# Optimization experiments

Hardware: AMD Instinct MI355X
Metric: run time of the kernel (lower is better)

Reference implementation:

```python
import jax, jax.numpy as jnp
import numpy as np

N_HEADS = 4
EMBED = 128
KDIM = EMBED // N_HEADS  # 32
FFH = 512
EPS = 1e-5


def _layer_norm_global(x):
    # PDP-N2S 'layer' norm: normalize over ALL of (nodes, features) per sample,
    # torch .var() is unbiased (ddof=1)
    mean = jnp.mean(x, axis=(1, 2), keepdims=True)
    var = jnp.var(x, axis=(1, 2), keepdims=True, ddof=1)
    return (x - mean) / jnp.sqrt(var + EPS)


def setup_inputs() -> dict:
    key = jax.random.key(0)
    ks = jax.random.split(key, 12)
    B, N = 8, 1024
    u = lambda k, shape, fan: jax.random.uniform(k, shape, jnp.float32, -1.0 / np.sqrt(fan), 1.0 / np.sqrt(fan))
    return {
        "input1": jax.random.normal(ks[0], (B, N, EMBED), jnp.float32),
        "input2": jax.random.normal(ks[1], (N_HEADS, B, N, N), jnp.float32),
        "W_query": u(ks[2], (N_HEADS, EMBED, KDIM), KDIM),
        "W_key": u(ks[3], (N_HEADS, EMBED, KDIM), KDIM),
        "W_val": u(ks[4], (N_HEADS, EMBED, KDIM), KDIM),
        "W_out": u(ks[5], (N_HEADS, KDIM, EMBED), EMBED),
        "Ws1": u(ks[6], (8, 8), 8),   # score_aggr layer 1, stored (in,out)
        "bs1": u(ks[7], (8,), 8),
        "Ws2": u(ks[8], (8, 4), 4),
        "bs2": u(ks[9], (4,), 4),
        "W_ff1": u(ks[10], (EMBED, FFH), FFH),  # stored (in,out), no bias
        "W_ff2": u(ks[11], (FFH, EMBED), EMBED),
    }


def reference(input1, input2, W_query, W_key, W_val, W_out, Ws1, bs1, Ws2, bs2, W_ff1, W_ff2):
    h = input1  # [B,N,E]
    # per-head projections: [H,B,N,K]
    Q = jnp.einsum('bne,hek->hbnk', h, W_query)
    K = jnp.einsum('bne,hek->hbnk', h, W_key)
    V = jnp.einsum('bne,hek->hbnk', h, W_val)
    # compatibility: 4 QK^T heads concatenated with 4 auxiliary score heads -> [8,B,N,N]
    compat = jnp.concatenate([jnp.einsum('hbnk,hbmk->hbnm', Q, K), input2], axis=0)
    # tiny per-element MLP across the 8-channel head axis -> 4 heads
    x = jnp.moveaxis(compat, 0, -1)                     # [B,N,N,8]
    x = jax.nn.relu(x @ Ws1 + bs1) @ Ws2 + bs2          # [B,N,N,4]
    attn = jax.nn.softmax(jnp.moveaxis(x, -1, 0), axis=-1)  # [4,B,N,N]
    heads = jnp.einsum('hbnm,hbmk->hbnk', attn, V)      # [H,B,N,K]
    out = jnp.einsum('hbnk,hke->bne', heads, W_out)     # [B,N,E]
    out1 = _layer_norm_global(out + h)
    # FF sublayer + norm
    ff = jax.nn.relu(out1 @ W_ff1) @ W_ff2
    out1 = _layer_norm_global(ff + out1)
    return (out1, input2)
```

## Files before the change

kernel.cpp:

```cpp
#include <hip/hip_runtime.h>
#include <hip/hip_bf16.h>

typedef __hip_bfloat16 bf16;

static constexpr int HN  = 4;
static constexpr int NB  = 8;
static constexpr int SEQ = 1024;
static constexpr int EMB = 128;
static constexpr int KD  = 32;
static constexpr int FFH = 512;
static constexpr int ROWS = NB * SEQ;
static constexpr float EPS = 1e-5f;

__device__ __forceinline__ float b2f(bf16 x){ return __bfloat162float(x); }

__device__ __forceinline__ float ldx(const void* p, size_t i, int f32){
    return f32 ? ((const float*)p)[i] : b2f(((const bf16*)p)[i]);
}

__device__ __forceinline__ float probe_max(const unsigned int* w, int nwords, int t){
    float mx = 0.f;
    for (int i = t; i < nwords; i += 256) {
        float v = fabsf(__uint_as_float(w[i] << 16));
        if (!(v <= 1e4f)) v = 1e30f;
        mx = fmaxf(mx, v);
    }
    return mx;
}

__global__ __launch_bounds__(256) void detect_kernel(
    const unsigned int* in1, const unsigned int* in2,
    const unsigned int* wq,  const unsigned int* wk, const unsigned int* wv,
    const unsigned int* wo,  const unsigned int* ws1, const unsigned int* bs1,
    const unsigned int* ws2, const unsigned int* bs2,
    const unsigned int* wf1, const unsigned int* wf2, int* __restrict__ flags)
{
    __shared__ float red[4];
    const int b = blockIdx.x, t = threadIdx.x;
    float mx = 0.f;
    if      (b == 0) mx = probe_max(in1, 4096, t);
    else if (b == 1) mx = probe_max(in2, 4096, t);
    else if (b == 2) mx = probe_max(wq, 4096, t);
    else if (b == 3) mx = probe_max(wk, 4096, t);
    else if (b == 4) mx = probe_max(wv, 4096, t);
    else if (b == 5) mx = probe_max(wo, 4096, t);
    else if (b == 6) {
        mx = fmaxf(probe_max(ws1, 32, t), probe_max(bs1, 4, t));
        mx = fmaxf(mx, fmaxf(probe_max(ws2, 16, t), probe_max(bs2, 2, t)));
    }
    else if (b == 7) mx = probe_max(wf1, 4096, t);
    else             mx = probe_max(wf2, 4096, t);

    #pragma unroll
    for (int off = 32; off >= 1; off >>= 1) mx = fmaxf(mx, __shfl_xor(mx, off));
    if ((t & 63) == 0) red[t >> 6] = mx;
    __syncthreads();
    if (t == 0) {
        mx = fmaxf(fmaxf(red[0], red[1]), fmaxf(red[2], red[3]));
        flags[b] = (mx > 1e4f) ? 1 : 0;
    }
}

__global__ __launch_bounds__(256) void convert_kernel(
    const void* in1, const void* Wq, const void* Wk, const void* Wv, const void* Wo,
    const void* Ws1, const void* bs1, const void* Ws2, const void* bs2,
    const void* Wf1, const void* Wf2,
    float* __restrict__ h32, float* __restrict__ Wt, float* __restrict__ Wot,
    float* __restrict__ W1t, float* __restrict__ W2t, float* __restrict__ mlp32,
    const int* __restrict__ flags)
{
    int gid = blockIdx.x * 256 + threadIdx.x;
    if (gid < 262144) {
        if (flags[0]) {
            ((float4*)h32)[gid] = ((const float4*)in1)[gid];
        } else {
            const bf16* p = (const bf16*)in1 + (size_t)gid * 4;
            h32[gid*4+0] = b2f(p[0]); h32[gid*4+1] = b2f(p[1]);
            h32[gid*4+2] = b2f(p[2]); h32[gid*4+3] = b2f(p[3]);
        }
        return;
    }
    int r = gid - 262144;
    if (r < 49152) {
        int mat = r >> 14, q = r & 16383;
        int h = q >> 12, k = (q >> 7) & 31, e = q & 127;
        const void* W = (mat == 0) ? Wq : (mat == 1) ? Wk : Wv;
        Wt[r] = ldx(W, (size_t)(h*EMB + e)*KD + k, flags[2+mat]);
        return;
    }
    r -= 49152;
    if (r < 16384) {
        int e = r >> 7, hk = r & 127;
        Wot[r] = ldx(Wo, (size_t)hk*EMB + e, flags[5]);
        return;
    }
    r -= 16384;
    if (r < 65536) {
        int f = r >> 7, e = r & 127;
        W1t[r] = ldx(Wf1, (size_t)e*FFH + f, flags[7]);
        return;
    }
    r -= 65536;
    if (r < 65536) {
        int e = r >> 9, f = r & 511;
        W2t[r] = ldx(Wf2, (size_t)f*EMB + e, flags[8]);
        return;
    }
    r -= 65536;
    if (r < 108) {
        const int fm = flags[6];
        float v;
        if (r < 64)       { int j = r >> 3, i = r & 7; v = ldx(Ws1, i*8 + j, fm); }
        else if (r < 72)  v = ldx(bs1, r - 64, fm);
        else if (r < 104) v = ldx(Ws2, r - 72, fm);
        else              v = ldx(bs2, r - 104, fm);
        mlp32[r] = v;
    }
}

__global__ __launch_bounds__(256) void qkv_kernel(
    const float* __restrict__ h32, const float* __restrict__ Wt,
    float* __restrict__ Q32, float* __restrict__ Kt32, float* __restrict__ Vt32)
{
    __shared__ float hl[128 * 132];
    const int t   = threadIdx.x;
    const int bid = blockIdx.x;
    const int mat = bid >> 8;
    const int hh  = (bid >> 6) & 3;
    const int rt  = bid & 63;
    const int row0 = rt * 128;

    #pragma unroll
    for (int i = 0; i < 16; i++) {
        int idx = t + 256 * i;
        int r  = idx >> 5;
        int e4 = (idx & 31) * 4;
        float4 v = *reinterpret_cast<const float4*>(h32 + (size_t)(row0 + r) * EMB + e4);
        *reinterpret_cast<float4*>(&hl[r * 132 + e4]) = v;
    }
    __syncthreads();

    const int rq = t >> 3;
    const int kq = t & 7;
    const float* wbase = Wt + ((size_t)(mat * HN + hh) * KD + kq * 4) * EMB;
    float acc[4][4] = {};
    #pragma unroll 4
    for (int eq = 0; eq < 32; eq++) {
        float4 a0 = *reinterpret_cast<const float4*>(&hl[(rq*4+0)*132 + eq*4]);
        float4 a1 = *reinterpret_cast<const float4*>(&hl[(rq*4+1)*132 + eq*4]);
        float4 a2 = *reinterpret_cast<const float4*>(&hl[(rq*4+2)*132 + eq*4]);
        float4 a3 = *reinterpret_cast<const float4*>(&hl[(rq*4+3)*132 + eq*4]);
        float4 w0 = *reinterpret_cast<const float4*>(wbase + 0*EMB + eq*4);
        float4 w1 = *reinterpret_cast<const float4*>(wbase + 1*EMB + eq*4);
        float4 w2 = *reinterpret_cast<const float4*>(wbase + 2*EMB + eq*4);
        float4 w3 = *reinterpret_cast<const float4*>(wbase + 3*EMB + eq*4);
        #pragma unroll
        for (int kk = 0; kk < 4; kk++) {
            float4 w = (kk==0)?w0:(kk==1)?w1:(kk==2)?w2:w3;
            acc[0][kk] += a0.x*w.x + a0.y*w.y + a0.z*w.z + a0.w*w.w;
            acc[1][kk] += a1.x*w.x + a1.y*w.y + a1.z*w.z + a1.w*w.w;
            acc[2][kk] += a2.x*w.x + a2.y*w.y + a2.z*w.z + a2.w*w.w;
            acc[3][kk] += a3.x*w.x + a3.y*w.y + a3.z*w.z + a3.w*w.w;
        }
    }

    if (mat == 0) {
        #pragma unroll
        for (int r = 0; r < 4; r++) {
            float4 v = { acc[r][0], acc[r][1], acc[r][2], acc[r][3] };
            *reinterpret_cast<float4*>(Q32 + ((size_t)hh*ROWS + row0 + rq*4 + r)*KD + kq*4) = v;
        }
    } else {
        float* out = (mat == 1) ? Kt32 : Vt32;
        int bb = row0 >> 10;
        int n0 = (row0 & 1023) + rq * 4;
        #pragma unroll
        for (int kk = 0; kk < 4; kk++) {
            float4 v = { acc[0][kk], acc[1][kk], acc[2][kk], acc[3][kk] };
            *reinterpret_cast<float4*>(out + ((size_t)(hh*NB + bb)*KD + kq*4 + kk)*SEQ + n0) = v;
        }
    }
}

#define P1_CHUNK(KC)                                                           \
    {                                                                          \
        float q0[16], q1[16];                                                  \
        _Pragma("unroll")                                                      \
        for (int i = 0; i < 4; i++) {                                          \
            float4 a = *reinterpret_cast<const float4*>(&qld[w][0][(KC)*16 + i*4]); \
            float4 c = *reinterpret_cast<const float4*>(&qld[w][1][(KC)*16 + i*4]); \
            q0[4*i+0]=a.x; q0[4*i+1]=a.y; q0[4*i+2]=a.z; q0[4*i+3]=a.w;        \
            q1[4*i+0]=c.x; q1[4*i+1]=c.y; q1[4*i+2]=c.z; q1[4*i+3]=c.w;        \
        }                                                                      \
        _Pragma("unroll 2")                                                    \
        for (int mc = 0; mc < 4; mc++) {                                       \
            const int m = mc*256 + l*4;                                        \
            float4 s0, s1;                                                     \
            if (KC) {                                                          \
                s0 = *reinterpret_cast<const float4*>(&sz[(w*2+0)*SEQ + m]);   \
                s1 = *reinterpret_cast<const float4*>(&sz[(w*2+1)*SEQ + m]);   \
            } else {                                                           \
                s0 = make_float4(0.f,0.f,0.f,0.f);                             \
                s1 = make_float4(0.f,0.f,0.f,0.f);                             \
            }                                                                  \
            _Pragma("unroll")                                                  \
            for (int k = 0; k < 16; k++) {                                     \
                float4 kv = *reinterpret_cast<const float4*>(kb + (size_t)((KC)*16 + k)*SEQ + m); \
                s0.x += q0[k]*kv.x; s0.y += q0[k]*kv.y; s0.z += q0[k]*kv.z; s0.w += q0[k]*kv.w; \
                s1.x += q1[k]*kv.x; s1.y += q1[k]*kv.y; s1.z += q1[k]*kv.z; s1.w += q1[k]*kv.w; \
            }                                                                  \
            *reinterpret_cast<float4*>(&sz[(w*2+0)*SEQ + m]) = s0;             \
            *reinterpret_cast<float4*>(&sz[(w*2+1)*SEQ + m]) = s1;             \
        }                                                                      \
    }

#define MLP_ROW(R, V0, V1, V2, V3)                                            \
    {                                                                          \
        float x0[8], x1[8], x2[8], x3[8];                                      \
        _Pragma("unroll")                                                      \
        for (int h = 0; h < 4; h++) {                                          \
            float4 s4 = *reinterpret_cast<const float4*>(&sz[(h*2+(R))*SEQ + m0]); \
            x0[h]=s4.x; x1[h]=s4.y; x2[h]=s4.z; x3[h]=s4.w;                    \
        }                                                                      \
        x0[4]=(V0).x; x1[4]=(V0).y; x2[4]=(V0).z; x3[4]=(V0).w;                \
        x0[5]=(V1).x; x1[5]=(V1).y; x2[5]=(V1).z; x3[5]=(V1).w;                \
        x0[6]=(V2).x; x1[6]=(V2).y; x2[6]=(V2).z; x3[6]=(V2).w;                \
        x0[7]=(V3).x; x1[7]=(V3).y; x2[7]=(V3).z; x3[7]=(V3).w;                \
        float zc[4][4];                                                        \
        _Pragma("unroll")                                                      \
        for (int m = 0; m < 4; m++) {                                          \
            _Pragma("unroll")                                                  \
            for (int c = 0; c < 4; c++) zc[m][c] = wm[104 + c];                \
        }                                                                      \
        _Pragma("unroll")                                                      \
        for (int j = 0; j < 8; j++) {                                          \
            float4 wa = *reinterpret_cast<const float4*>(&wm[j*8]);            \
            float4 wb = *reinterpret_cast<const float4*>(&wm[j*8+4]);          \
            float b1j = wm[64 + j];                                            \
            float4 w2v = *reinterpret_cast<const float4*>(&wm[72 + j*4]);      \
            float y0 = b1j + x0[0]*wa.x + x0[1]*wa.y + x0[2]*wa.z + x0[3]*wa.w \
                           + x0[4]*wb.x + x0[5]*wb.y + x0[6]*wb.z + x0[7]*wb.w;\
            float y1 = b1j + x1[0]*wa.x + x1[1]*wa.y + x1[2]*wa.z + x1[3]*wa.w \
                           + x1[4]*wb.x + x1[5]*wb.y + x1[6]*wb.z + x1[7]*wb.w;\
            float y2 = b1j + x2[0]*wa.x + x2[1]*wa.y + x2[2]*wa.z + x2[3]*wa.w \
                           + x2[4]*wb.x + x2[5]*wb.y + x2[6]*wb.z + x2[7]*wb.w;\
            float y3 = b1j + x3[0]*wa.x + x3[1]*wa.y + x3[2]*wa.z + x3[3]*wa.w \
                           + x3[4]*wb.x + x3[5]*wb.y + x3[6]*wb.z + x3[7]*wb.w;\
            y0 = fmaxf(y0, 0.f); y1 = fmaxf(y1, 0.f);                          \
            y2 = fmaxf(y2, 0.f); y3 = fmaxf(y3, 0.f);                          \
            zc[0][0] += y0*w2v.x; zc[0][1] += y0*w2v.y; zc[0][2] += y0*w2v.z; zc[0][3] += y0*w2v.w; \
            zc[1][0] += y1*w2v.x; zc[1][1] += y1*w2v.y; zc[1][2] += y1*w2v.z; zc[1][3] += y1*w2v.w; \
            zc[2][0] += y2*w2v.x; zc[2][1] += y2*w2v.y; zc[2][2] += y2*w2v.z; zc[2][3] += y2*w2v.w; \
            zc[3][0] += y3*w2v.x; zc[3][1] += y3*w2v.y; zc[3][2] += y3*w2v.z; zc[3][3] += y3*w2v.w; \
        }                                                                      \
        _Pragma("unroll")                                                      \
        for (int c = 0; c < 4; c++)                                            \
            *reinterpret_cast<float4*>(&sz[(c*2 + (R))*SEQ + m0]) =            \
                make_float4(zc[0][c], zc[1][c], zc[2][c], zc[3][c]);           \
    }

__global__ __launch_bounds__(256, 2) void attn_kernel(
    const float* __restrict__ Q32, const float* __restrict__ Kt32,
    const float* __restrict__ Vt32, const void* __restrict__ in2,
    const float* __restrict__ mlp, float* __restrict__ heads,
    const int* __restrict__ flags)
{
    __shared__ float sz[8704];
    __shared__ float qld[HN][2][KD];
    __shared__ float wm[108];
    __shared__ float invs[2][HN];

    const int t = threadIdx.x;
    const int wg   = (blockIdx.x & 7) * 512 + (blockIdx.x >> 3);
    const int row0 = wg * 2;
    const int b    = row0 >> 10;
    const int n0   = row0 & (SEQ - 1);
    const int m0   = t * 4;
    const int f2   = flags[1];
    const int w    = t >> 6, l = t & 63;

    { int h = t >> 6, r = (t >> 5) & 1, k = t & 31;
      qld[h][r][k] = Q32[((size_t)h*ROWS + row0 + r)*KD + k]; }
    if (t < 108) wm[t] = mlp[t];

    auto ld2 = [&](int c, int r) -> float4 {
        size_t base = ((size_t)(c*NB + b)*SEQ + (n0 + r))*SEQ + m0;
        if (f2) return *reinterpret_cast<const float4*>((const float*)in2 + base);
        ushort4 u = *reinterpret_cast<const ushort4*>((const ushort*)in2 + base);
        return make_float4(
            __uint_as_float((unsigned)u.x << 16), __uint_as_float((unsigned)u.y << 16),
            __uint_as_float((unsigned)u.z << 16), __uint_as_float((unsigned)u.w << 16));
    };
    float4 iA0 = ld2(0,0), iA1 = ld2(1,0), iA2 = ld2(2,0), iA3 = ld2(3,0);
    float4 iB0 = ld2(0,1), iB1 = ld2(1,1), iB2 = ld2(2,1), iB3 = ld2(3,1);
    __syncthreads();

    {
        const float* kb = Kt32 + ((size_t)(w*NB + b)*KD)*SEQ;
        P1_CHUNK(0)
        P1_CHUNK(1)
    }
    __syncthreads();

    MLP_ROW(0, iA0, iA1, iA2, iA3)
    MLP_ROW(1, iB0, iB1, iB2, iB3)
    __syncthreads();

    float p0[16], p1[16];
    {
        #pragma unroll
        for (int i = 0; i < 4; i++) {
            float4 a = *reinterpret_cast<const float4*>(&sz[(w*2+0)*SEQ + i*256 + l*4]);
            float4 c = *reinterpret_cast<const float4*>(&sz[(w*2+1)*SEQ + i*256 + l*4]);
            p0[4*i+0]=a.x; p0[4*i+1]=a.y; p0[4*i+2]=a.z; p0[4*i+3]=a.w;
            p1[4*i+0]=c.x; p1[4*i+1]=c.y; p1[4*i+2]=c.z; p1[4*i+3]=c.w;
        }
        float mx0 = -1e30f, mx1 = -1e30f;
        #pragma unroll
        for (int i = 0; i < 16; i++) { mx0 = fmaxf(mx0, p0[i]); mx1 = fmaxf(mx1, p1[i]); }
        #pragma unroll
        for (int off = 32; off >= 1; off >>= 1) {
            mx0 = fmaxf(mx0, __shfl_xor(mx0, off));
            mx1 = fmaxf(mx1, __shfl_xor(mx1, off));
        }
        float s0 = 0.f, s1 = 0.f;
        #pragma unroll
        for (int i = 0; i < 16; i++) {
            p0[i] = __expf(p0[i] - mx0); s0 += p0[i];
            p1[i] = __expf(p1[i] - mx1); s1 += p1[i];
        }
        #pragma unroll
        for (int off = 32; off >= 1; off >>= 1) { s0 += __shfl_xor(s0, off); s1 += __shfl_xor(s1, off); }
        if (l == 0) { invs[0][w] = 1.f / s0; invs[1][w] = 1.f / s1; }
    }
    __syncthreads();

    #pragma unroll 1
    for (int kh = 0; kh < 2; kh++) {
        float o0[16], o1[16];
        #pragma unroll
        for (int i = 0; i < 16; i++) { o0[i] = 0.f; o1[i] = 0.f; }
        const float* vb = Vt32 + ((size_t)(w*NB + b)*KD + kh*16)*SEQ + l*4;
        #pragma unroll
        for (int k16 = 0; k16 < 16; k16++) {
            const float* vk = vb + (size_t)k16*SEQ;
            float4 v0 = *reinterpret_cast<const float4*>(vk + 0*256);
            float4 v1 = *reinterpret_cast<const float4*>(vk + 1*256);
            float4 v2 = *reinterpret_cast<const float4*>(vk + 2*256);
            float4 v3 = *reinterpret_cast<const float4*>(vk + 3*256);
            o0[k16] = p0[ 0]*v0.x + p0[ 1]*v0.y + p0[ 2]*v0.z + p0[ 3]*v0.w
                    + p0[ 4]*v1.x + p0[ 5]*v1.y + p0[ 6]*v1.z + p0[ 7]*v1.w
                    + p0[ 8]*v2.x + p0[ 9]*v2.y + p0[10]*v2.z + p0[11]*v2.w
                    + p0[12]*v3.x + p0[13]*v3.y + p0[14]*v3.z + p0[15]*v3.w;
            o1[k16] = p1[ 0]*v0.x + p1[ 1]*v0.y + p1[ 2]*v0.z + p1[ 3]*v0.w
                    + p1[ 4]*v1.x + p1[ 5]*v1.y + p1[ 6]*v1.z + p1[ 7]*v1.w
                    + p1[ 8]*v2.x + p1[ 9]*v2.y + p1[10]*v2.z + p1[11]*v2.w
                    + p1[12]*v3.x + p1[13]*v3.y + p1[14]*v3.z + p1[15]*v3.w;
        }
        #pragma unroll
        for (int i = 0; i < 16; i++) { o0[i] += __shfl_xor(o0[i], 32); o1[i] += __shfl_xor(o1[i], 32); }
        if (l < 32) {
            float* rr = &sz[(w*32 + l)*68 + kh*16];
            #pragma unroll
            for (int i = 0; i < 4; i++) {
                *reinterpret_cast<float4*>(rr + i*4)      = make_float4(o0[4*i], o0[4*i+1], o0[4*i+2], o0[4*i+3]);
                *reinterpret_cast<float4*>(rr + 32 + i*4) = make_float4(o1[4*i], o1[4*i+1], o1[4*i+2], o1[4*i+3]);
            }
        }
    }
    __syncthreads();
    {
        int r = t >> 7, h = (t >> 5) & 3, k = t & 31;
        float acc = 0.f;
        #pragma unroll 8
        for (int l2 = 0; l2 < 32; l2++) acc += sz[(h*32 + l2)*68 + r*32 + k];
        heads[((size_t)h*ROWS + row0 + r)*KD + k] = acc * invs[r][h];
    }
}

__global__ __launch_bounds__(256) void outproj_kernel(
    const float* __restrict__ heads, const float* __restrict__ Wot,
    const float* __restrict__ h32, float* __restrict__ outp,
    float* __restrict__ ps, float* __restrict__ pq)
{
    const int gid = blockIdx.x * 256 + threadIdx.x;
    const int row = gid >> 7, e = gid & 127;
    float acc = h32[gid];
    #pragma unroll
    for (int h = 0; h < HN; h++) {
        const float4* hp = reinterpret_cast<const float4*>(heads + ((size_t)h*ROWS + row)*KD);
        const float4* wp = reinterpret_cast<const float4*>(Wot + (size_t)e*EMB + h*KD);
        #pragma unroll
        for (int i = 0; i < 8; i++) {
            float4 a = hp[i], w = wp[i];
            acc += a.x*w.x + a.y*w.y + a.z*w.z + a.w*w.w;
        }
    }
    outp[gid] = acc;
    float s = acc, q = acc * acc;
    #pragma unroll
    for (int off = 32; off >= 1; off >>= 1) { s += __shfl_xor(s, off); q += __shfl_xor(q, off); }
    __shared__ float ls[4], lq[4];
    if ((threadIdx.x & 63) == 0) { ls[threadIdx.x >> 6] = s; lq[threadIdx.x >> 6] = q; }
    __syncthreads();
    if (threadIdx.x == 0) {
        ps[blockIdx.x] = ls[0] + ls[1] + ls[2] + ls[3];
        pq[blockIdx.x] = lq[0] + lq[1] + lq[2] + lq[3];
    }
}

__global__ __launch_bounds__(256) void stats_kernel(
    const float* __restrict__ ps, const float* __restrict__ pq,
    float* __restrict__ stats, int per_b, float M)
{
    int b = blockIdx.x, t = threadIdx.x;
    float s = 0.f, q = 0.f;
    for (int i = t; i < per_b; i += 256) { s += ps[b * per_b + i]; q += pq[b * per_b + i]; }
    #pragma unroll
    for (int off = 32; off >= 1; off >>= 1) { s += __shfl_xor(s, off); q += __shfl_xor(q, off); }
    __shared__ float ls[4], lq[4];
    if ((t & 63) == 0) { ls[t >> 6] = s; lq[t >> 6] = q; }
    __syncthreads();
    if (t == 0) {
        s = ls[0] + ls[1] + ls[2] + ls[3];
        q = lq[0] + lq[1] + lq[2] + lq[3];
        float mean = s / M;
        float var = (q - s * s / M) / (M - 1.0f);
        stats[2 * b] = mean;
        stats[2 * b + 1] = 1.0f / sqrtf(var + EPS);
    }
}

__global__ __launch_bounds__(256) void ff_kernel(
    const float* __restrict__ outp, const float* __restrict__ stats,
    const float* __restrict__ W1t, const float* __restrict__ W2t,
    float* __restrict__ outp2, float* __restrict__ ps, float* __restrict__ pq)
{
    __shared__ float xr[8][EMB];
    __shared__ float hid[8][FFH];
    __shared__ float rs[4], rq[4];
    const int t = threadIdx.x;
    const int row0 = blockIdx.x * 8;
    const int b = row0 >> 10;
    const float mean = stats[2*b], rstd = stats[2*b+1];

    {
        float4 x4 = *reinterpret_cast<const float4*>(outp + (size_t)row0*EMB + t*4);
        int rr = t >> 5, cc = (t*4) & 127;
        xr[rr][cc+0] = (x4.x - mean)*rstd; xr[rr][cc+1] = (x4.y - mean)*rstd;
        xr[rr][cc+2] = (x4.z - mean)*rstd; xr[rr][cc+3] = (x4.w - mean)*rstd;
    }
    __syncthreads();

    {
        const float4* w0 = reinterpret_cast<const float4*>(W1t + (size_t)t * EMB);
        const float4* w1 = reinterpret_cast<const float4*>(W1t + (size_t)(t + 256) * EMB);
        float a[2][8] = {};
        #pragma unroll 8
        for (int i = 0; i < 32; i++) {
            float4 wa = w0[i], wb = w1[i];
            #pragma unroll
            for (int r = 0; r < 8; r++) {
                float4 x = *reinterpret_cast<const float4*>(&xr[r][i*4]);
                a[0][r] += wa.x*x.x + wa.y*x.y + wa.z*x.z + wa.w*x.w;
                a[1][r] += wb.x*x.x + wb.y*x.y + wb.z*x.z + wb.w*x.w;
            }
        }
        #pragma unroll
        for (int r = 0; r < 8; r++) {
            hid[r][t]       = fmaxf(a[0][r], 0.f);
            hid[r][t + 256] = fmaxf(a[1][r], 0.f);
        }
    }
    __syncthreads();

    const int e = t >> 1, half = t & 1;
    float acc[8] = {};
    {
        const float4* wvp = reinterpret_cast<const float4*>(W2t + (size_t)e*FFH + half*256);
        #pragma unroll 8
        for (int i = 0; i < 64; i++) {
            float4 w = wvp[i];
            int fb = half*256 + i*4;
            #pragma unroll
            for (int r = 0; r < 8; r++) {
                float4 h4 = *reinterpret_cast<const float4*>(&hid[r][fb]);
                acc[r] += w.x*h4.x + w.y*h4.y + w.z*h4.z + w.w*h4.w;
            }
        }
    }
    #pragma unroll
    for (int r = 0; r < 8; r++) acc[r] += __shfl_xor(acc[r], 1);
    float s = 0.f, q = 0.f;
    if (half == 0) {
        #pragma unroll
        for (int r = 0; r < 8; r++) {
            float v = acc[r] + xr[r][e];
            outp2[(size_t)(row0 + r)*EMB + e] = v;
            s += v; q += v * v;
        }
    }
    #pragma unroll
    for (int off = 32; off >= 1; off >>= 1) { s += __shfl_xor(s, off); q += __shfl_xor(q, off); }
    if ((t & 63) == 0) { rs[t >> 6] = s; rq[t >> 6] = q; }
    __syncthreads();
    if (t == 0) {
        ps[blockIdx.x] = rs[0] + rs[1] + rs[2] + rs[3];
        pq[blockIdx.x] = rq[0] + rq[1] + rq[2] + rq[3];
    }
}

__global__ __launch_bounds__(256) void final_kernel(
    const float* __restrict__ in, const float* __restrict__ stats, float* __restrict__ out)
{
    int gid = blockIdx.x * 256 + threadIdx.x;
    int b = gid >> 17;
    out[gid] = (in[gid] - stats[2 * b]) * stats[2 * b + 1];
}

__global__ __launch_bounds__(256) void copy2_kernel(
    const void* __restrict__ in, uint4* __restrict__ out, const int* __restrict__ flags)
{
    const int f_2 = flags[1];
    size_t gid = (size_t)blockIdx.x * 256 + threadIdx.x;
    if (f_2) {
        out[gid] = ((const uint4*)in)[gid];
    } else {
        const bf16* p = (const bf16*)in + gid * 4;
        float4 v = { b2f(p[0]), b2f(p[1]), b2f(p[2]), b2f(p[3]) };
        out[gid] = *(const uint4*)&v;
    }
}

extern "C" void kernel_launch(void* const* d_in, const int* in_sizes, int n_in,
                              void* d_out, int out_size, void* d_ws, size_t ws_size,
                              hipStream_t stream)
{
    const void* input1 = d_in[0];
    const void* input2 = d_in[1];
    const void* Wq  = d_in[2];
    const void* Wk  = d_in[3];
    const void* Wv  = d_in[4];
    const void* Wo  = d_in[5];
    const void* Ws1 = d_in[6];
    const void* bs1 = d_in[7];
    const void* Ws2 = d_in[8];
    const void* bs2 = d_in[9];
    const void* Wf1 = d_in[10];
    const void* Wf2 = d_in[11];

    float* out1 = (float*)d_out;
    float* out2 = (float*)d_out + (size_t)ROWS * EMB;

    char* sb = (char*)out2;
    float* Q32   = (float*)(sb);
    float* Kt32  = (float*)(sb + (4u  << 20));
    float* Vt32  = (float*)(sb + (8u  << 20));
    float* heads = (float*)(sb + (12u << 20));
    float* outp  = (float*)(sb + (16u << 20));
    float* outp2 = (float*)(sb + (20u << 20));
    float* h32   = (float*)(sb + (24u << 20));
    float* Wt    = (float*)(sb + (28u << 20));
    float* Wot   = (float*)(sb + (28u << 20) + 0x30000);
    float* W1t   = (float*)(sb + (28u << 20) + 0x40000);
    float* W2t   = (float*)(sb + (28u << 20) + 0x80000);
    float* mlp32 = (float*)(sb + (28u << 20) + 0xC0000);
    float* ps    = (float*)(sb + (28u << 20) + 0xC1000);
    float* pq    = (float*)(sb + (28u << 20) + 0xC5000);
    float* stats = (float*)(sb + (28u << 20) + 0xC9000);
    float* stats2= (float*)(sb + (28u << 20) + 0xC9100);
    int*   flags = (int*)  (sb + (28u << 20) + 0xC9200);

    const float M = (float)(SEQ * EMB);

    hipLaunchKernelGGL(detect_kernel, dim3(9), dim3(256), 0, stream,
                       (const unsigned int*)input1, (const unsigned int*)input2,
                       (const unsigned int*)Wq, (const unsigned int*)Wk,
                       (const unsigned int*)Wv, (const unsigned int*)Wo,
                       (const unsigned int*)Ws1, (const unsigned int*)bs1,
                       (const unsigned int*)Ws2, (const unsigned int*)bs2,
                       (const unsigned int*)Wf1, (const unsigned int*)Wf2, flags);
    hipLaunchKernelGGL(convert_kernel, dim3(1793), dim3(256), 0, stream,
                       input1, Wq, Wk, Wv, Wo, Ws1, bs1, Ws2, bs2, Wf1, Wf2,
                       h32, Wt, Wot, W1t, W2t, mlp32, flags);
    hipLaunchKernelGGL(qkv_kernel, dim3(768), dim3(256), 0, stream,
                       h32, Wt, Q32, Kt32, Vt32);
    hipLaunchKernelGGL(attn_kernel, dim3(ROWS / 2), dim3(256), 0, stream,
                       Q32, Kt32, Vt32, input2, mlp32, heads, flags);
    hipLaunchKernelGGL(outproj_kernel, dim3(ROWS * EMB / 256), dim3(256), 0, stream,
                       heads, Wot, h32, outp, ps, pq);
    hipLaunchKernelGGL(stats_kernel, dim3(NB), dim3(256), 0, stream,
                       ps, pq, stats, 512, M);
    hipLaunchKernelGGL(ff_kernel, dim3(ROWS / 8), dim3(256), 0, stream,
                       outp, stats, W1t, W2t, outp2, ps, pq);
    hipLaunchKernelGGL(stats_kernel, dim3(NB), dim3(256), 0, stream,
                       ps, pq, stats2, 128, M);
    hipLaunchKernelGGL(final_kernel, dim3(ROWS * EMB / 256), dim3(256), 0, stream,
                       outp2, stats2, out1);
    hipLaunchKernelGGL(copy2_kernel, dim3(ROWS * SEQ * HN / 4 / 256), dim3(256), 0, stream,
                       input2, (uint4*)out2, flags);
}
```

Baseline: 620.3 us.

## Store K and V in bf16 and read input1 directly, dropping h32 staging

The K and V projections are now written as bf16 instead of fp32, halving the bytes the attention kernel reads in its QK and PV loops and widening them back to float on load. The separate conversion pass that copied input1 into an fp32 buffer is removed. The QKV and out-projection kernels now read input1 directly, converting it as needed based on the dtype flag. This cuts memory traffic and one large pass but rounds K and V to bf16, adding numerical error.

```diff
diff --git a/kernel.cpp b/kernel.cpp
--- a/kernel.cpp
+++ b/kernel.cpp
@@ -2,6 +2,7 @@
 #include <hip/hip_bf16.h>
 
 typedef __hip_bfloat16 bf16;
+typedef unsigned short ushort_t;
 
 static constexpr int HN  = 4;
 static constexpr int NB  = 8;
@@ -13,6 +14,11 @@
 static constexpr float EPS = 1e-5f;
 
 __device__ __forceinline__ float b2f(bf16 x){ return __bfloat162float(x); }
+__device__ __forceinline__ float u2f(unsigned short u){ return __uint_as_float((unsigned)u << 16); }
+__device__ __forceinline__ unsigned short f2bu(float x){
+    bf16 b = __float2bfloat16(x);
+    return *reinterpret_cast<unsigned short*>(&b);
+}
 
 __device__ __forceinline__ float ldx(const void* p, size_t i, int f32){
     return f32 ? ((const float*)p)[i] : b2f(((const bf16*)p)[i]);
@@ -62,25 +68,14 @@
 }
 
 __global__ __launch_bounds__(256) void convert_kernel(
-    const void* in1, const void* Wq, const void* Wk, const void* Wv, const void* Wo,
+    const void* Wq, const void* Wk, const void* Wv, const void* Wo,
     const void* Ws1, const void* bs1, const void* Ws2, const void* bs2,
     const void* Wf1, const void* Wf2,
-    float* __restrict__ h32, float* __restrict__ Wt, float* __restrict__ Wot,
+    float* __restrict__ Wt, float* __restrict__ Wot,
     float* __restrict__ W1t, float* __restrict__ W2t, float* __restrict__ mlp32,
     const int* __restrict__ flags)
 {
-    int gid = blockIdx.x * 256 + threadIdx.x;
-    if (gid < 262144) {
-        if (flags[0]) {
-            ((float4*)h32)[gid] = ((const float4*)in1)[gid];
-        } else {
-            const bf16* p = (const bf16*)in1 + (size_t)gid * 4;
-            h32[gid*4+0] = b2f(p[0]); h32[gid*4+1] = b2f(p[1]);
-            h32[gid*4+2] = b2f(p[2]); h32[gid*4+3] = b2f(p[3]);
-        }
-        return;
-    }
-    int r = gid - 262144;
+    int r = blockIdx.x * 256 + threadIdx.x;
     if (r < 49152) {
         int mat = r >> 14, q = r & 16383;
         int h = q >> 12, k = (q >> 7) & 31, e = q & 127;
@@ -119,8 +114,9 @@
 }
 
 __global__ __launch_bounds__(256) void qkv_kernel(
-    const float* __restrict__ h32, const float* __restrict__ Wt,
-    float* __restrict__ Q32, float* __restrict__ Kt32, float* __restrict__ Vt32)
+    const void* __restrict__ in1, const float* __restrict__ Wt,
+    float* __restrict__ Q32, ushort_t* __restrict__ Ktb, ushort_t* __restrict__ Vtb,
+    const int* __restrict__ flags)
 {
     __shared__ float hl[128 * 132];
     const int t   = threadIdx.x;
@@ -129,13 +125,20 @@
     const int hh  = (bid >> 6) & 3;
     const int rt  = bid & 63;
     const int row0 = rt * 128;
+    const int f_h = flags[0];
 
     #pragma unroll
     for (int i = 0; i < 16; i++) {
         int idx = t + 256 * i;
         int r  = idx >> 5;
         int e4 = (idx & 31) * 4;
-        float4 v = *reinterpret_cast<const float4*>(h32 + (size_t)(row0 + r) * EMB + e4);
+        float4 v;
+        if (f_h) {
+            v = *reinterpret_cast<const float4*>((const float*)in1 + (size_t)(row0 + r) * EMB + e4);
+        } else {
+            ushort4 u = *reinterpret_cast<const ushort4*>((const ushort_t*)in1 + (size_t)(row0 + r) * EMB + e4);
+            v = make_float4(u2f(u.x), u2f(u.y), u2f(u.z), u2f(u.w));
+        }
         *reinterpret_cast<float4*>(&hl[r * 132 + e4]) = v;
     }
     __syncthreads();
@@ -171,13 +174,13 @@
             *reinterpret_cast<float4*>(Q32 + ((size_t)hh*ROWS + row0 + rq*4 + r)*KD + kq*4) = v;
         }
     } else {
-        float* out = (mat == 1) ? Kt32 : Vt32;
+        ushort_t* out = (mat == 1) ? Ktb : Vtb;
         int bb = row0 >> 10;
         int n0 = (row0 & 1023) + rq * 4;
         #pragma unroll
         for (int kk = 0; kk < 4; kk++) {
-            float4 v = { acc[0][kk], acc[1][kk], acc[2][kk], acc[3][kk] };
-            *reinterpret_cast<float4*>(out + ((size_t)(hh*NB + bb)*KD + kq*4 + kk)*SEQ + n0) = v;
+            ushort4 u = { f2bu(acc[0][kk]), f2bu(acc[1][kk]), f2bu(acc[2][kk]), f2bu(acc[3][kk]) };
+            *reinterpret_cast<ushort4*>(out + ((size_t)(hh*NB + bb)*KD + kq*4 + kk)*SEQ + n0) = u;
         }
     }
 }
@@ -205,9 +208,10 @@
             }                                                                  \
             _Pragma("unroll")                                                  \
             for (int k = 0; k < 16; k++) {                                     \
-                float4 kv = *reinterpret_cast<const float4*>(kb + (size_t)((KC)*16 + k)*SEQ + m); \
-                s0.x += q0[k]*kv.x; s0.y += q0[k]*kv.y; s0.z += q0[k]*kv.z; s0.w += q0[k]*kv.w; \
-                s1.x += q1[k]*kv.x; s1.y += q1[k]*kv.y; s1.z += q1[k]*kv.z; s1.w += q1[k]*kv.w; \
+                ushort4 ku = *reinterpret_cast<const ushort4*>(kb + (size_t)((KC)*16 + k)*SEQ + m); \
+                float kx = u2f(ku.x), ky = u2f(ku.y), kz = u2f(ku.z), kw = u2f(ku.w); \
+                s0.x += q0[k]*kx; s0.y += q0[k]*ky; s0.z += q0[k]*kz; s0.w += q0[k]*kw; \
+                s1.x += q1[k]*kx; s1.y += q1[k]*ky; s1.z += q1[k]*kz; s1.w += q1[k]*kw; \
             }                                                                  \
             *reinterpret_cast<float4*>(&sz[(w*2+0)*SEQ + m]) = s0;             \
             *reinterpret_cast<float4*>(&sz[(w*2+1)*SEQ + m]) = s1;             \
@@ -260,8 +264,8 @@
     }
 
 __global__ __launch_bounds__(256, 2) void attn_kernel(
-    const float* __restrict__ Q32, const float* __restrict__ Kt32,
-    const float* __restrict__ Vt32, const void* __restrict__ in2,
+    const float* __restrict__ Q32, const ushort_t* __restrict__ Ktb,
+    const ushort_t* __restrict__ Vtb, const void* __restrict__ in2,
     const float* __restrict__ mlp, float* __restrict__ heads,
     const int* __restrict__ flags)
 {
@@ -286,17 +290,15 @@
     auto ld2 = [&](int c, int r) -> float4 {
         size_t base = ((size_t)(c*NB + b)*SEQ + (n0 + r))*SEQ + m0;
         if (f2) return *reinterpret_cast<const float4*>((const float*)in2 + base);
-        ushort4 u = *reinterpret_cast<const ushort4*>((const ushort*)in2 + base);
-        return make_float4(
-            __uint_as_float((unsigned)u.x << 16), __uint_as_float((unsigned)u.y << 16),
-            __uint_as_float((unsigned)u.z << 16), __uint_as_float((unsigned)u.w << 16));
+        ushort4 u = *reinterpret_cast<const ushort4*>((const ushort_t*)in2 + base);
+        return make_float4(u2f(u.x), u2f(u.y), u2f(u.z), u2f(u.w));
     };
     float4 iA0 = ld2(0,0), iA1 = ld2(1,0), iA2 = ld2(2,0), iA3 = ld2(3,0);
     float4 iB0 = ld2(0,1), iB1 = ld2(1,1), iB2 = ld2(2,1), iB3 = ld2(3,1);
     __syncthreads();
 
     {
-        const float* kb = Kt32 + ((size_t)(w*NB + b)*KD)*SEQ;
+        const ushort_t* kb = Ktb + ((size_t)(w*NB + b)*KD)*SEQ;
         P1_CHUNK(0)
         P1_CHUNK(1)
     }
@@ -340,22 +342,26 @@
         float o0[16], o1[16];
         #pragma unroll
         for (int i = 0; i < 16; i++) { o0[i] = 0.f; o1[i] = 0.f; }
-        const float* vb = Vt32 + ((size_t)(w*NB + b)*KD + kh*16)*SEQ + l*4;
+        const ushort_t* vb = Vtb + ((size_t)(w*NB + b)*KD + kh*16)*SEQ + l*4;
         #pragma unroll
         for (int k16 = 0; k16 < 16; k16++) {
-            const float* vk = vb + (size_t)k16*SEQ;
-            float4 v0 = *reinterpret_cast<const float4*>(vk + 0*256);
-            float4 v1 = *reinterpret_cast<const float4*>(vk + 1*256);
-            float4 v2 = *reinterpret_cast<const float4*>(vk + 2*256);
-            float4 v3 = *reinterpret_cast<const float4*>(vk + 3*256);
-            o0[k16] = p0[ 0]*v0.x + p0[ 1]*v0.y + p0[ 2]*v0.z + p0[ 3]*v0.w
-                    + p0[ 4]*v1.x + p0[ 5]*v1.y + p0[ 6]*v1.z + p0[ 7]*v1.w
-                    + p0[ 8]*v2.x + p0[ 9]*v2.y + p0[10]*v2.z + p0[11]*v2.w
-                    + p0[12]*v3.x + p0[13]*v3.y + p0[14]*v3.z + p0[15]*v3.w;
-            o1[k16] = p1[ 0]*v0.x + p1[ 1]*v0.y + p1[ 2]*v0.z + p1[ 3]*v0.w
-                    + p1[ 4]*v1.x + p1[ 5]*v1.y + p1[ 6]*v1.z + p1[ 7]*v1.w
-                    + p1[ 8]*v2.x + p1[ 9]*v2.y + p1[10]*v2.z + p1[11]*v2.w
-                    + p1[12]*v3.x + p1[13]*v3.y + p1[14]*v3.z + p1[15]*v3.w;
+            const ushort_t* vk = vb + (size_t)k16*SEQ;
+            ushort4 u0 = *reinterpret_cast<const ushort4*>(vk + 0*256);
+            ushort4 u1 = *reinterpret_cast<const ushort4*>(vk + 1*256);
+            ushort4 u2 = *reinterpret_cast<const ushort4*>(vk + 2*256);
+            ushort4 u3 = *reinterpret_cast<const ushort4*>(vk + 3*256);
+            float v00=u2f(u0.x), v01=u2f(u0.y), v02=u2f(u0.z), v03=u2f(u0.w);
+            float v10=u2f(u1.x), v11=u2f(u1.y), v12=u2f(u1.z), v13=u2f(u1.w);
+            float v20=u2f(u2.x), v21=u2f(u2.y), v22=u2f(u2.z), v23=u2f(u2.w);
+            float v30=u2f(u3.x), v31=u2f(u3.y), v32=u2f(u3.z), v33=u2f(u3.w);
+            o0[k16] = p0[ 0]*v00 + p0[ 1]*v01 + p0[ 2]*v02 + p0[ 3]*v03
+                    + p0[ 4]*v10 + p0[ 5]*v11 + p0[ 6]*v12 + p0[ 7]*v13
+                    + p0[ 8]*v20 + p0[ 9]*v21 + p0[10]*v22 + p0[11]*v23
+                    + p0[12]*v30 + p0[13]*v31 + p0[14]*v32 + p0[15]*v33;
+            o1[k16] = p1[ 0]*v00 + p1[ 1]*v01 + p1[ 2]*v02 + p1[ 3]*v03
+                    + p1[ 4]*v10 + p1[ 5]*v11 + p1[ 6]*v12 + p1[ 7]*v13
+                    + p1[ 8]*v20 + p1[ 9]*v21 + p1[10]*v22 + p1[11]*v23
+                    + p1[12]*v30 + p1[13]*v31 + p1[14]*v32 + p1[15]*v33;
         }
         #pragma unroll
         for (int i = 0; i < 16; i++) { o0[i] += __shfl_xor(o0[i], 32); o1[i] += __shfl_xor(o1[i], 32); }
@@ -380,12 +386,12 @@
 
 __global__ __launch_bounds__(256) void outproj_kernel(
     const float* __restrict__ heads, const float* __restrict__ Wot,
-    const float* __restrict__ h32, float* __restrict__ outp,
-    float* __restrict__ ps, float* __restrict__ pq)
+    const void* __restrict__ in1, float* __restrict__ outp,
+    float* __restrict__ ps, float* __restrict__ pq, const int* __restrict__ flags)
 {
     const int gid = blockIdx.x * 256 + threadIdx.x;
     const int row = gid >> 7, e = gid & 127;
-    float acc = h32[gid];
+    float acc = ldx(in1, gid, flags[0]);
     #pragma unroll
     for (int h = 0; h < HN; h++) {
         const float4* hp = reinterpret_cast<const float4*>(heads + ((size_t)h*ROWS + row)*KD);
@@ -553,13 +559,12 @@
     float* out2 = (float*)d_out + (size_t)ROWS * EMB;
 
     char* sb = (char*)out2;
-    float* Q32   = (float*)(sb);
-    float* Kt32  = (float*)(sb + (4u  << 20));
-    float* Vt32  = (float*)(sb + (8u  << 20));
+    float*    Q32   = (float*)(sb);
+    ushort_t* Ktb   = (ushort_t*)(sb + (4u  << 20));
+    ushort_t* Vtb   = (ushort_t*)(sb + (8u  << 20));
     float* heads = (float*)(sb + (12u << 20));
     float* outp  = (float*)(sb + (16u << 20));
     float* outp2 = (float*)(sb + (20u << 20));
-    float* h32   = (float*)(sb + (24u << 20));
     float* Wt    = (float*)(sb + (28u << 20));
     float* Wot   = (float*)(sb + (28u << 20) + 0x30000);
     float* W1t   = (float*)(sb + (28u << 20) + 0x40000);
@@ -580,15 +585,15 @@
                        (const unsigned int*)Ws1, (const unsigned int*)bs1,
                        (const unsigned int*)Ws2, (const unsigned int*)bs2,
                        (const unsigned int*)Wf1, (const unsigned int*)Wf2, flags);
-    hipLaunchKernelGGL(convert_kernel, dim3(1793), dim3(256), 0, stream,
-                       input1, Wq, Wk, Wv, Wo, Ws1, bs1, Ws2, bs2, Wf1, Wf2,
-                       h32, Wt, Wot, W1t, W2t, mlp32, flags);
+    hipLaunchKernelGGL(convert_kernel, dim3(769), dim3(256), 0, stream,
+                       Wq, Wk, Wv, Wo, Ws1, bs1, Ws2, bs2, Wf1, Wf2,
+                       Wt, Wot, W1t, W2t, mlp32, flags);
     hipLaunchKernelGGL(qkv_kernel, dim3(768), dim3(256), 0, stream,
-                       h32, Wt, Q32, Kt32, Vt32);
+                       input1, Wt, Q32, Ktb, Vtb, flags);
     hipLaunchKernelGGL(attn_kernel, dim3(ROWS / 2), dim3(256), 0, stream,
-                       Q32, Kt32, Vt32, input2, mlp32, heads, flags);
+                       Q32, Ktb, Vtb, input2, mlp32, heads, flags);
     hipLaunchKernelGGL(outproj_kernel, dim3(ROWS * EMB / 256), dim3(256), 0, stream,
-                       heads, Wot, h32, outp, ps, pq);
+                       heads, Wot, input1, outp, ps, pq, flags);
     hipLaunchKernelGGL(stats_kernel, dim3(NB), dim3(256), 0, stream,
                        ps, pq, stats, 512, M);
     hipLaunchKernelGGL(ff_kernel, dim3(ROWS / 8), dim3(256), 0, stream,
```

Result: no change. 630.4 us (+1.6%).
